# Kernel optimization log

Measured on AMD Instinct MI355X. Metric: run time of the kernel, lower is better.

Reference implementation:

```python
import jax, jax.numpy as jnp
import numpy as np

N_NODES = 20000
N_EDGES = 120000
N_GRAPHS = 512
F_IN = 300
NHID = 256
NHID_FF = 256
NOUT = 768
SLOPE = 0.2
EPS = 1e-16


def _p(key, shape, scale=0.05):
    return jax.random.normal(key, shape, dtype=jnp.float32) * scale


def setup_inputs() -> dict:
    key = jax.random.key(0)
    ks = jax.random.split(key, 24)
    inp = {
        "x": jax.random.normal(ks[0], (N_NODES, F_IN), dtype=jnp.float32),
        "edge_index": jax.random.randint(ks[1], (2, N_EDGES), 0, N_NODES, dtype=jnp.int64) if False else jax.random.randint(ks[1], (2, N_EDGES), 0, N_NODES).astype(jnp.int32),
        "batch": jnp.sort(jax.random.randint(ks[2], (N_NODES,), 0, N_GRAPHS)).astype(jnp.int32),
        # conv1: in=300 -> heads=4, C=256, concat
        "c1_wl": _p(ks[3], (4 * NHID, F_IN)),
        "c1_wr": _p(ks[4], (4 * NHID, F_IN)),
        "c1_att": _p(ks[5], (4, NHID)),
        "c1_b": jnp.zeros((4 * NHID,), jnp.float32),
        # conv2: in=1024 -> heads=4, C=256, concat
        "c2_wl": _p(ks[6], (4 * NHID, 4 * NHID)),
        "c2_wr": _p(ks[7], (4 * NHID, 4 * NHID)),
        "c2_att": _p(ks[8], (4, NHID)),
        "c2_b": jnp.zeros((4 * NHID,), jnp.float32),
        # conv3: in=1024 -> heads=6, C=256, mean (concat=False)
        "c3_wl": _p(ks[9], (6 * NHID_FF, 4 * NHID)),
        "c3_wr": _p(ks[10], (6 * NHID_FF, 4 * NHID)),
        "c3_att": _p(ks[11], (6, NHID_FF)),
        "c3_b": jnp.zeros((NHID_FF,), jnp.float32),
        # post-process MLP
        "fp1_w": _p(ks[12], (NHID_FF, NHID_FF)),
        "fp1_b": jnp.zeros((NHID_FF,), jnp.float32),
        "fp2_w": _p(ks[13], (NOUT, NHID_FF)),
        "fp2_b": jnp.zeros((NOUT,), jnp.float32),
    }
    return inp


def gatv2(x, src, dst, wl, wr, att, b, concat):
    """GATv2Conv (PyG semantics, eval mode): lin_l on source, lin_r on target,
    score = att . leaky_relu(xl_j + xr_i), segment softmax over dst, aggregate xl_j."""
    n = x.shape[0]
    H, C = att.shape
    xl = (x @ wl.T).reshape(n, H, C)
    xr = (x @ wr.T).reshape(n, H, C)
    s = xl[src] + xr[dst]                                   # [E,H,C] gather
    s = jnp.where(s > 0, s, SLOPE * s)                      # leaky_relu
    scores = jnp.einsum("ehc,hc->eh", s, att)               # [E,H]
    mx = jax.ops.segment_max(scores, dst, num_segments=n)   # [N,H]
    ex = jnp.exp(scores - mx[dst])
    denom = jax.ops.segment_sum(ex, dst, num_segments=n)
    alpha = ex / (denom[dst] + EPS)                         # [E,H]
    out = jax.ops.segment_sum(alpha[:, :, None] * xl[src], dst, num_segments=n)  # [N,H,C]
    out = out.reshape(n, H * C) if concat else out.mean(axis=1)
    return out + b


def reference(x, edge_index, batch, c1_wl, c1_wr, c1_att, c1_b,
              c2_wl, c2_wr, c2_att, c2_b, c3_wl, c3_wr, c3_att, c3_b,
              fp1_w, fp1_b, fp2_w, fp2_b):
    n = x.shape[0]
    # PyG GATv2Conv defaults add_self_loops=True
    loops = jnp.arange(n, dtype=edge_index.dtype)
    src = jnp.concatenate([edge_index[0], loops])
    dst = jnp.concatenate([edge_index[1], loops])

    h = jax.nn.elu(gatv2(x, src, dst, c1_wl, c1_wr, c1_att, c1_b, concat=True))
    h = jax.nn.elu(gatv2(h, src, dst, c2_wl, c2_wr, c2_att, c2_b, concat=True))
    h = gatv2(h, src, dst, c3_wl, c3_wr, c3_att, c3_b, concat=False)

    # F.normalize(p=2, dim=-1), torch eps=1e-12
    norm = jnp.linalg.norm(h, axis=-1, keepdims=True)
    h = h / jnp.maximum(norm, 1e-12)

    # global_mean_pool over `batch`
    sums = jax.ops.segment_sum(h, batch, num_segments=N_GRAPHS)
    cnts = jax.ops.segment_sum(jnp.ones((n,), h.dtype), batch, num_segments=N_GRAPHS)
    pooled = sums / jnp.maximum(cnts, 1.0)[:, None]

    h = jax.nn.relu(pooled @ fp1_w.T + fp1_b)
    return h @ fp2_w.T + fp2_b
```

## Files before the change

### kernel.cpp

```cpp
#include <hip/hip_runtime.h>

typedef _Float16 h16;
typedef _Float16 h16x4 __attribute__((ext_vector_type(4)));
typedef _Float16 h16x8 __attribute__((ext_vector_type(8)));
typedef float f32x4 __attribute__((ext_vector_type(4)));

static constexpr int NN   = 20000;
static constexpr int NPAD = 20096;
static constexpr int NE0  = 120000;
static constexpr int NE   = 140000;
static constexpr int NG   = 512;
static constexpr int FIN  = 300;
static constexpr int K1P  = 320;
static constexpr int CD   = 256;
static constexpr float SLOPE = 0.2f;

#define GLDS16(gsrc, ldst)                                                              \
  __builtin_amdgcn_global_load_lds(                                                    \
      (const __attribute__((address_space(1))) unsigned int*)(gsrc),                    \
      (__attribute__((address_space(3))) unsigned int*)(ldst), 16, 0, 0)

__global__ __launch_bounds__(256) void fill_x_kernel(const float* __restrict__ x, h16* __restrict__ a1) {
  int r = blockIdx.x;
  for (int c = threadIdx.x; c < K1P; c += 256) {
    float v = (r < NN && c < FIN) ? x[(size_t)r * FIN + c] : 0.f;
    a1[(size_t)r * K1P + c] = (h16)v;
  }
}

__global__ __launch_bounds__(256) void conv_w2_kernel(const float* __restrict__ wl, const float* __restrict__ wr,
                                                      h16* __restrict__ o, int rows, int cols, int colsp) {
  int r = blockIdx.x;
  const float* s = (r < rows) ? (wl + (size_t)r * cols) : (wr + (size_t)(r - rows) * cols);
  for (int c = threadIdx.x; c < colsp; c += 256) {
    float v = (c < cols) ? s[c] : 0.f;
    o[(size_t)r * colsp + c] = (h16)v;
  }
}

__global__ __launch_bounds__(256) void build_edges_kernel(const int* __restrict__ ei,
                                                          int* __restrict__ src, int* __restrict__ dst) {
  int e = blockIdx.x * 256 + threadIdx.x;
  if (e >= NE) return;
  if (e < NE0) { src[e] = ei[e]; dst[e] = ei[NE0 + e]; }
  else         { src[e] = e - NE0; dst[e] = e - NE0; }
}

__global__ __launch_bounds__(256) void deg_kernel(const int* __restrict__ dst, int* __restrict__ deg) {
  int e = blockIdx.x * 256 + threadIdx.x;
  if (e < NE) atomicAdd(&deg[dst[e]], 1);
}

__global__ __launch_bounds__(1024) void scan_kernel(const int* __restrict__ deg, int* __restrict__ rowptr) {
  __shared__ int b0[1024], b1[1024];
  __shared__ int carry;
  int t = threadIdx.x;
  if (t == 0) carry = 0;
  __syncthreads();
  for (int base = 0; base < NN; base += 1024) {
    int x = (base + t < NN) ? deg[base + t] : 0;
    b0[t] = x;
    __syncthreads();
    int* cur = b0; int* nxt = b1;
    for (int off = 1; off < 1024; off <<= 1) {
      int v = cur[t];
      if (t >= off) v += cur[t - off];
      nxt[t] = v;
      __syncthreads();
      int* tmp = cur; cur = nxt; nxt = tmp;
    }
    if (base + t < NN) rowptr[base + t] = carry + cur[t] - x;
    __syncthreads();
    if (t == 0) carry += cur[1023];
    __syncthreads();
  }
  if (t == 0) rowptr[NN] = carry;
}

__global__ __launch_bounds__(256) void scatter_kernel(const int* __restrict__ src, const int* __restrict__ dst,
                                                      const int* __restrict__ rowptr, int* __restrict__ cursor,
                                                      int* __restrict__ esrc) {
  int e = blockIdx.x * 256 + threadIdx.x;
  if (e >= NE) return;
  int d = dst[e];
  int pos = rowptr[d] + atomicAdd(&cursor[d], 1);
  esrc[pos] = src[e];
}

__global__ __launch_bounds__(256) void gemm_kernel(const h16* __restrict__ A, const h16* __restrict__ B,
                                                   h16* __restrict__ Co, int K, int Nw, int ntN) {
  __shared__ __align__(16) h16 As[128 * 32];
  __shared__ __align__(16) h16 Bs[128 * 32];
  int nwg = gridDim.x;
  int q = nwg >> 3, r = nwg & 7;
  int xc = blockIdx.x & 7, idx = blockIdx.x >> 3;
  int logical = (xc < r ? xc * (q + 1) : r * (q + 1) + (xc - r) * q) + idx;
  int tm = (logical / ntN) * 128, tn = (logical % ntN) * 128;

  int tid = threadIdx.x, w = tid >> 6, lane = tid & 63;
  int wm = (w >> 1) * 64, wn = (w & 1) * 64;
  const h16* gA = A + (size_t)(tm + w * 16 + (lane >> 2)) * K + (lane & 3) * 8;
  const h16* gB = B + (size_t)(tn + w * 16 + (lane >> 2)) * K + (lane & 3) * 8;
  h16* lA0 = As + w * 512;
  h16* lA1 = As + 2048 + w * 512;
  h16* lB0 = Bs + w * 512;
  h16* lB1 = Bs + 2048 + w * 512;
  const size_t rowskip = (size_t)64 * K;
  int lrow = lane & 15, kg = (lane >> 4) * 8;

  f32x4 acc[4][4] = {};
  for (int k0 = 0; k0 < K; k0 += 32) {
    __syncthreads();
    GLDS16(gA + k0, lA0);
    GLDS16(gA + rowskip + k0, lA1);
    GLDS16(gB + k0, lB0);
    GLDS16(gB + rowskip + k0, lB1);
    __syncthreads();
    h16x8 af[4], bf[4];
#pragma unroll
    for (int i = 0; i < 4; i++) af[i] = *(const h16x8*)&As[(wm + i * 16 + lrow) * 32 + kg];
#pragma unroll
    for (int j = 0; j < 4; j++) bf[j] = *(const h16x8*)&Bs[(wn + j * 16 + lrow) * 32 + kg];
#pragma unroll
    for (int i = 0; i < 4; i++)
#pragma unroll
      for (int j = 0; j < 4; j++)
        acc[i][j] = __builtin_amdgcn_mfma_f32_16x16x32_f16(af[i], bf[j], acc[i][j], 0, 0, 0);
  }
  int cr = (lane >> 4) * 4, cc = lane & 15;
#pragma unroll
  for (int i = 0; i < 4; i++)
#pragma unroll
    for (int j = 0; j < 4; j++) {
      size_t base = (size_t)(tm + wm + i * 16 + cr) * Nw + (tn + wn + j * 16 + cc);
#pragma unroll
      for (int qq = 0; qq < 4; qq++) Co[base + (size_t)qq * Nw] = (h16)acc[i][j][qq];
    }
}

template <int H, int MODE>
__global__ __launch_bounds__(64 * H) void sagg_kernel(
    const h16* __restrict__ X, const int* __restrict__ rowptr, const int* __restrict__ esrc,
    const float* __restrict__ att, const float* __restrict__ bias,
    h16* __restrict__ outA, const int* __restrict__ batch,
    float* __restrict__ pooled, int* __restrict__ cnt) {
  constexpr int HC = H * CD, S = 2 * HC;
  int n = blockIdx.x;
  int tid = threadIdx.x, w = tid >> 6, lane = tid & 63;
  int cb = w * CD + lane * 4;

  float4 aw4 = *(const float4*)(att + cb);
  const float* aw = (const float*)&aw4;
  h16x4 xr4 = *(const h16x4*)(X + (size_t)n * S + HC + cb);
  float xr0 = (float)xr4[0], xr1 = (float)xr4[1], xr2 = (float)xr4[2], xr3 = (float)xr4[3];

  int beg = rowptr[n], end = rowptr[n + 1];
  float m = -1e30f, s = 0.f;
  float a0 = 0.f, a1 = 0.f, a2 = 0.f, a3 = 0.f;
  for (int i = beg; i < end; ++i) {
    int j = esrc[i];
    h16x4 xl4 = *(const h16x4*)(X + (size_t)j * S + cb);
    float x0 = (float)xl4[0], x1 = (float)xl4[1], x2 = (float)xl4[2], x3 = (float)xl4[3];
    float v0 = x0 + xr0, v1 = x1 + xr1, v2 = x2 + xr2, v3 = x3 + xr3;
    v0 = v0 > 0.f ? v0 : SLOPE * v0;
    v1 = v1 > 0.f ? v1 : SLOPE * v1;
    v2 = v2 > 0.f ? v2 : SLOPE * v2;
    v3 = v3 > 0.f ? v3 : SLOPE * v3;
    float p = v0 * aw[0] + v1 * aw[1] + v2 * aw[2] + v3 * aw[3];
    p += __shfl_xor(p, 32); p += __shfl_xor(p, 16); p += __shfl_xor(p, 8);
    p += __shfl_xor(p, 4);  p += __shfl_xor(p, 2);  p += __shfl_xor(p, 1);
    float nm = fmaxf(m, p);
    float f = __expf(m - nm), we = __expf(p - nm);
    s = s * f + we;
    a0 = a0 * f + we * x0; a1 = a1 * f + we * x1;
    a2 = a2 * f + we * x2; a3 = a3 * f + we * x3;
    m = nm;
  }
  float inv = 1.f / (s + 1e-16f);

  if (MODE == 0) {
    float o0 = a0 * inv + bias[cb + 0];
    float o1 = a1 * inv + bias[cb + 1];
    float o2 = a2 * inv + bias[cb + 2];
    float o3 = a3 * inv + bias[cb + 3];
    o0 = o0 > 0.f ? o0 : expm1f(o0);
    o1 = o1 > 0.f ? o1 : expm1f(o1);
    o2 = o2 > 0.f ? o2 : expm1f(o2);
    o3 = o3 > 0.f ? o3 : expm1f(o3);
    h16x4 ov = {(h16)o0, (h16)o1, (h16)o2, (h16)o3};
    *(h16x4*)(outA + (size_t)n * HC + cb) = ov;
  } else {
    __shared__ float sh[HC];
    __shared__ float red[H];
    float4 nv = {a0 * inv, a1 * inv, a2 * inv, a3 * inv};
    *(float4*)&sh[cb] = nv;
    __syncthreads();
    float mv = 0.f;
    if (tid < CD) {
#pragma unroll
      for (int h = 0; h < H; h++) mv += sh[h * CD + tid];
      mv = mv * (1.f / H) + bias[tid];
    }
    float ss = (tid < CD) ? mv * mv : 0.f;
    ss += __shfl_xor(ss, 32); ss += __shfl_xor(ss, 16); ss += __shfl_xor(ss, 8);
    ss += __shfl_xor(ss, 4);  ss += __shfl_xor(ss, 2);  ss += __shfl_xor(ss, 1);
    if (lane == 0) red[w] = ss;
    __syncthreads();
    float tot = 0.f;
#pragma unroll
    for (int h = 0; h < H; h++) tot += red[h];
    float scale = 1.f / fmaxf(sqrtf(tot), 1e-12f);
    int g = batch[n];
    if (tid < CD) atomicAdd(&pooled[(size_t)g * CD + tid], mv * scale);
    if (tid == 0) atomicAdd(&cnt[g], 1);
  }
}

__global__ __launch_bounds__(256) void pool_div_kernel(float* __restrict__ pooled, const int* __restrict__ cnt) {
  int g = blockIdx.x, t = threadIdx.x;
  pooled[(size_t)g * CD + t] /= fmaxf((float)cnt[g], 1.f);
}

__global__ __launch_bounds__(256) void mlp1_kernel(const float* __restrict__ pooled, const float* __restrict__ w,
                                                   const float* __restrict__ b, float* __restrict__ hid) {
  __shared__ float xs[CD];
  int g = blockIdx.x, t = threadIdx.x;
  xs[t] = pooled[(size_t)g * CD + t];
  __syncthreads();
  float acc = b[t];
  for (int k = 0; k < CD; ++k) acc += xs[k] * w[(size_t)t * CD + k];
  hid[(size_t)g * CD + t] = fmaxf(acc, 0.f);
}

__global__ __launch_bounds__(256) void mlp2_kernel(const float* __restrict__ hid, const float* __restrict__ w,
                                                   const float* __restrict__ b, float* __restrict__ out) {
  __shared__ float xs[CD];
  int g = blockIdx.x, t = threadIdx.x;
  xs[t] = hid[(size_t)g * CD + t];
  __syncthreads();
  for (int o = t; o < 768; o += 256) {
    float acc = b[o];
    for (int k = 0; k < CD; ++k) acc += xs[k] * w[(size_t)o * CD + k];
    out[(size_t)g * 768 + o] = acc;
  }
}

extern "C" void kernel_launch(void* const* d_in, const int* in_sizes, int n_in,
                              void* d_out, int out_size, void* d_ws, size_t ws_size,
                              hipStream_t stream) {
  const float* x      = (const float*)d_in[0];
  const int*   ei     = (const int*)d_in[1];
  const int*   batch  = (const int*)d_in[2];
  const float* c1_wl  = (const float*)d_in[3];
  const float* c1_wr  = (const float*)d_in[4];
  const float* c1_att = (const float*)d_in[5];
  const float* c1_b   = (const float*)d_in[6];
  const float* c2_wl  = (const float*)d_in[7];
  const float* c2_wr  = (const float*)d_in[8];
  const float* c2_att = (const float*)d_in[9];
  const float* c2_b   = (const float*)d_in[10];
  const float* c3_wl  = (const float*)d_in[11];
  const float* c3_wr  = (const float*)d_in[12];
  const float* c3_att = (const float*)d_in[13];
  const float* c3_b   = (const float*)d_in[14];
  const float* fp1_w  = (const float*)d_in[15];
  const float* fp1_b  = (const float*)d_in[16];
  const float* fp2_w  = (const float*)d_in[17];
  const float* fp2_b  = (const float*)d_in[18];

  char* p = (char*)d_ws;
  size_t off = 0;
  auto alloc = [&](size_t b) { void* r = p + off; off += (b + 255) & ~(size_t)255; return r; };
  h16*  A    = (h16*)alloc((size_t)NPAD * 1024 * 2);
  h16*  Xa   = (h16*)alloc((size_t)NPAD * 3072 * 2);
  h16*  Xb   = (h16*)alloc((size_t)NPAD * 2048 * 2);
  h16*  A1   = Xb;
  h16*  W1   = (h16*)alloc((size_t)2048 * K1P * 2);
  h16*  W2   = (h16*)alloc((size_t)2048 * 1024 * 2);
  h16*  W3   = (h16*)alloc((size_t)3072 * 1024 * 2);
  int*  srcA   = (int*)alloc((size_t)NE * 4);
  int*  dstA   = (int*)alloc((size_t)NE * 4);
  int*  esrc   = (int*)alloc((size_t)NE * 4);
  int*  deg    = (int*)alloc((size_t)NN * 4);
  int*  cursor = (int*)alloc((size_t)NN * 4);
  int*  rowptr = (int*)alloc((size_t)(NN + 1) * 4);
  float* pooled = (float*)alloc((size_t)NG * CD * 4);
  int*  cnt    = (int*)alloc((size_t)NG * 4);
  float* hid   = (float*)alloc((size_t)NG * CD * 4);

  hipMemsetAsync(deg, 0, (size_t)NN * 4, stream);
  hipMemsetAsync(cursor, 0, (size_t)NN * 4, stream);
  hipMemsetAsync(pooled, 0, (size_t)NG * CD * 4, stream);
  hipMemsetAsync(cnt, 0, (size_t)NG * 4, stream);

  fill_x_kernel<<<NPAD, 256, 0, stream>>>(x, A1);
  conv_w2_kernel<<<2048, 256, 0, stream>>>(c1_wl, c1_wr, W1, 1024, FIN, K1P);
  conv_w2_kernel<<<2048, 256, 0, stream>>>(c2_wl, c2_wr, W2, 1024, 1024, 1024);
  conv_w2_kernel<<<3072, 256, 0, stream>>>(c3_wl, c3_wr, W3, 1536, 1024, 1024);

  int eb = (NE + 255) / 256;
  build_edges_kernel<<<eb, 256, 0, stream>>>(ei, srcA, dstA);
  deg_kernel<<<eb, 256, 0, stream>>>(dstA, deg);
  scan_kernel<<<1, 1024, 0, stream>>>(deg, rowptr);
  scatter_kernel<<<eb, 256, 0, stream>>>(srcA, dstA, rowptr, cursor, esrc);

  gemm_kernel<<<157 * 16, 256, 0, stream>>>(A1, W1, Xa, K1P, 2048, 16);
  sagg_kernel<4, 0><<<NN, 256, 0, stream>>>(Xa, rowptr, esrc, c1_att, c1_b, A, nullptr, nullptr, nullptr);

  gemm_kernel<<<157 * 16, 256, 0, stream>>>(A, W2, Xb, 1024, 2048, 16);
  sagg_kernel<4, 0><<<NN, 256, 0, stream>>>(Xb, rowptr, esrc, c2_att, c2_b, A, nullptr, nullptr, nullptr);

  gemm_kernel<<<157 * 24, 256, 0, stream>>>(A, W3, Xa, 1024, 3072, 24);
  sagg_kernel<6, 1><<<NN, 384, 0, stream>>>(Xa, rowptr, esrc, c3_att, c3_b, nullptr, batch, pooled, cnt);

  pool_div_kernel<<<NG, 256, 0, stream>>>(pooled, cnt);
  mlp1_kernel<<<NG, 256, 0, stream>>>(pooled, fp1_w, fp1_b, hid);
  mlp2_kernel<<<NG, 256, 0, stream>>>(hid, fp2_w, fp2_b, (float*)d_out);
}
```

Measured before the change: 777.4 us.

## Use 256x256 double-buffered swizzled GEMM tiles and batch neighbor gathers in aggregation

Replaces the 128x128 single-buffered GEMM with a 256x256-tile, 512-thread kernel. It uses K-step 64, double-buffered LDS via global_load_lds, an XOR swizzle against bank conflicts, and explicit waitcnt and barrier control so loads overlap the MFMAs. Padding grows (K1P to 384, NPAD to 20224) to fit the larger tiles. The aggregation kernels now prefetch up to 8 neighbor indices and feature rows before the online-softmax loop, exposing memory-level parallelism in the edge gather. The larger tiles cut global and LDS traffic per MFMA but raise register and LDS pressure (128KB of LDS per block) and do extra padded work.

```diff
diff --git a/kernel.cpp b/kernel.cpp
--- a/kernel.cpp
+++ b/kernel.cpp
@@ -6,12 +6,12 @@
 typedef float f32x4 __attribute__((ext_vector_type(4)));
 
 static constexpr int NN   = 20000;
-static constexpr int NPAD = 20096;
+static constexpr int NPAD = 20224;
 static constexpr int NE0  = 120000;
 static constexpr int NE   = 140000;
 static constexpr int NG   = 512;
 static constexpr int FIN  = 300;
-static constexpr int K1P  = 320;
+static constexpr int K1P  = 384;
 static constexpr int CD   = 256;
 static constexpr float SLOPE = 0.2f;
 
@@ -87,51 +87,80 @@
   esrc[pos] = src[e];
 }
 
-__global__ __launch_bounds__(256) void gemm_kernel(const h16* __restrict__ A, const h16* __restrict__ B,
-                                                   h16* __restrict__ Co, int K, int Nw, int ntN) {
-  __shared__ __align__(16) h16 As[128 * 32];
-  __shared__ __align__(16) h16 Bs[128 * 32];
+__global__ __launch_bounds__(512, 2) void gemm256_kernel(const h16* __restrict__ A, const h16* __restrict__ B,
+                                                         h16* __restrict__ Co, int K, int Nw, int ntN) {
+  __shared__ __align__(16) h16 lds[4 * 16384];
   int nwg = gridDim.x;
   int q = nwg >> 3, r = nwg & 7;
   int xc = blockIdx.x & 7, idx = blockIdx.x >> 3;
   int logical = (xc < r ? xc * (q + 1) : r * (q + 1) + (xc - r) * q) + idx;
-  int tm = (logical / ntN) * 128, tn = (logical % ntN) * 128;
-
-  int tid = threadIdx.x, w = tid >> 6, lane = tid & 63;
-  int wm = (w >> 1) * 64, wn = (w & 1) * 64;
-  const h16* gA = A + (size_t)(tm + w * 16 + (lane >> 2)) * K + (lane & 3) * 8;
-  const h16* gB = B + (size_t)(tn + w * 16 + (lane >> 2)) * K + (lane & 3) * 8;
-  h16* lA0 = As + w * 512;
-  h16* lA1 = As + 2048 + w * 512;
-  h16* lB0 = Bs + w * 512;
-  h16* lB1 = Bs + 2048 + w * 512;
-  const size_t rowskip = (size_t)64 * K;
-  int lrow = lane & 15, kg = (lane >> 4) * 8;
-
-  f32x4 acc[4][4] = {};
-  for (int k0 = 0; k0 < K; k0 += 32) {
-    __syncthreads();
-    GLDS16(gA + k0, lA0);
-    GLDS16(gA + rowskip + k0, lA1);
-    GLDS16(gB + k0, lB0);
-    GLDS16(gB + rowskip + k0, lB1);
-    __syncthreads();
-    h16x8 af[4], bf[4];
-#pragma unroll
-    for (int i = 0; i < 4; i++) af[i] = *(const h16x8*)&As[(wm + i * 16 + lrow) * 32 + kg];
-#pragma unroll
-    for (int j = 0; j < 4; j++) bf[j] = *(const h16x8*)&Bs[(wn + j * 16 + lrow) * 32 + kg];
-#pragma unroll
-    for (int i = 0; i < 4; i++)
-#pragma unroll
-      for (int j = 0; j < 4; j++)
+  int tm = (logical / ntN) * 256, tn = (logical % ntN) * 256;
+
+  int tid = threadIdx.x;
+  int wv = tid >> 6, lane = tid & 63;
+  int wm = (wv >> 2) * 128, wn = (wv & 3) * 64;
+  int lrow = lane & 15, kq = lane >> 4, lr7 = lrow & 7;
+
+  int rowoff = tid >> 3;
+  int ug = ((tid & 7) ^ (rowoff & 7)) * 8;
+  int ldsoff = (tid >> 6) * 512;
+
+  const int NT = K >> 6;
+
+  auto STAGE = [&](int buf, int kt) {
+#pragma unroll
+    for (int j = 0; j < 4; ++j) {
+      GLDS16(A + (size_t)(tm + j * 64 + rowoff) * K + kt * 64 + ug,
+             &lds[(buf * 2 + 0) * 16384 + j * 4096 + ldsoff]);
+      GLDS16(B + (size_t)(tn + j * 64 + rowoff) * K + kt * 64 + ug,
+             &lds[(buf * 2 + 1) * 16384 + j * 4096 + ldsoff]);
+    }
+  };
+
+  STAGE(0, 0);
+  STAGE(1, 1);
+
+  f32x4 acc[8][4] = {};
+  for (int t = 0; t < NT; ++t) {
+    int b = t & 1;
+    if (t + 1 < NT) { asm volatile("s_waitcnt vmcnt(8)" ::: "memory"); }
+    else            { asm volatile("s_waitcnt vmcnt(0)" ::: "memory"); }
+    __builtin_amdgcn_s_barrier();
+
+    const h16* As_ = &lds[(b * 2 + 0) * 16384];
+    const h16* Bs_ = &lds[(b * 2 + 1) * 16384];
+    h16x8 af[8], bf[4];
+#pragma unroll
+    for (int i = 0; i < 8; ++i) af[i] = *(const h16x8*)&As_[(wm + i * 16 + lrow) * 64 + ((kq ^ lr7) * 8)];
+#pragma unroll
+    for (int j = 0; j < 4; ++j) bf[j] = *(const h16x8*)&Bs_[(wn + j * 16 + lrow) * 64 + ((kq ^ lr7) * 8)];
+#pragma unroll
+    for (int i = 0; i < 8; ++i)
+#pragma unroll
+      for (int j = 0; j < 4; ++j)
         acc[i][j] = __builtin_amdgcn_mfma_f32_16x16x32_f16(af[i], bf[j], acc[i][j], 0, 0, 0);
-  }
-  int cr = (lane >> 4) * 4, cc = lane & 15;
-#pragma unroll
-  for (int i = 0; i < 4; i++)
-#pragma unroll
-    for (int j = 0; j < 4; j++) {
+#pragma unroll
+    for (int i = 0; i < 8; ++i) af[i] = *(const h16x8*)&As_[(wm + i * 16 + lrow) * 64 + (((4 + kq) ^ lr7) * 8)];
+#pragma unroll
+    for (int j = 0; j < 4; ++j) bf[j] = *(const h16x8*)&Bs_[(wn + j * 16 + lrow) * 64 + (((4 + kq) ^ lr7) * 8)];
+    asm volatile("s_waitcnt lgkmcnt(0)" ::: "memory");
+    __builtin_amdgcn_sched_barrier(0);
+    __builtin_amdgcn_s_barrier();
+    if (t + 2 < NT) STAGE(b, t + 2);
+    __builtin_amdgcn_s_setprio(1);
+#pragma unroll
+    for (int i = 0; i < 8; ++i)
+#pragma unroll
+      for (int j = 0; j < 4; ++j)
+        acc[i][j] = __builtin_amdgcn_mfma_f32_16x16x32_f16(af[i], bf[j], acc[i][j], 0, 0, 0);
+    __builtin_amdgcn_s_setprio(0);
+  }
+
+  int cr = kq * 4, cc = lrow;
+#pragma unroll
+  for (int i = 0; i < 8; ++i)
+#pragma unroll
+    for (int j = 0; j < 4; ++j) {
       size_t base = (size_t)(tm + wm + i * 16 + cr) * Nw + (tn + wn + j * 16 + cc);
 #pragma unroll
       for (int qq = 0; qq < 4; qq++) Co[base + (size_t)qq * Nw] = (h16)acc[i][j][qq];
@@ -157,24 +186,36 @@
   int beg = rowptr[n], end = rowptr[n + 1];
   float m = -1e30f, s = 0.f;
   float a0 = 0.f, a1 = 0.f, a2 = 0.f, a3 = 0.f;
-  for (int i = beg; i < end; ++i) {
-    int j = esrc[i];
-    h16x4 xl4 = *(const h16x4*)(X + (size_t)j * S + cb);
-    float x0 = (float)xl4[0], x1 = (float)xl4[1], x2 = (float)xl4[2], x3 = (float)xl4[3];
-    float v0 = x0 + xr0, v1 = x1 + xr1, v2 = x2 + xr2, v3 = x3 + xr3;
-    v0 = v0 > 0.f ? v0 : SLOPE * v0;
-    v1 = v1 > 0.f ? v1 : SLOPE * v1;
-    v2 = v2 > 0.f ? v2 : SLOPE * v2;
-    v3 = v3 > 0.f ? v3 : SLOPE * v3;
-    float p = v0 * aw[0] + v1 * aw[1] + v2 * aw[2] + v3 * aw[3];
-    p += __shfl_xor(p, 32); p += __shfl_xor(p, 16); p += __shfl_xor(p, 8);
-    p += __shfl_xor(p, 4);  p += __shfl_xor(p, 2);  p += __shfl_xor(p, 1);
-    float nm = fmaxf(m, p);
-    float f = __expf(m - nm), we = __expf(p - nm);
-    s = s * f + we;
-    a0 = a0 * f + we * x0; a1 = a1 * f + we * x1;
-    a2 = a2 * f + we * x2; a3 = a3 * f + we * x3;
-    m = nm;
+  int i = beg;
+  while (i < end) {
+    int cn = end - i; if (cn > 8) cn = 8;
+    int js[8];
+    h16x4 xs[8];
+#pragma unroll
+    for (int k = 0; k < 8; ++k) js[k] = esrc[i + (k < cn ? k : cn - 1)];
+#pragma unroll
+    for (int k = 0; k < 8; ++k) xs[k] = *(const h16x4*)(X + (size_t)js[k] * S + cb);
+#pragma unroll
+    for (int k = 0; k < 8; ++k) {
+      if (k < cn) {
+        float x0 = (float)xs[k][0], x1 = (float)xs[k][1], x2 = (float)xs[k][2], x3 = (float)xs[k][3];
+        float v0 = x0 + xr0, v1 = x1 + xr1, v2 = x2 + xr2, v3 = x3 + xr3;
+        v0 = v0 > 0.f ? v0 : SLOPE * v0;
+        v1 = v1 > 0.f ? v1 : SLOPE * v1;
+        v2 = v2 > 0.f ? v2 : SLOPE * v2;
+        v3 = v3 > 0.f ? v3 : SLOPE * v3;
+        float p = v0 * aw[0] + v1 * aw[1] + v2 * aw[2] + v3 * aw[3];
+        p += __shfl_xor(p, 32); p += __shfl_xor(p, 16); p += __shfl_xor(p, 8);
+        p += __shfl_xor(p, 4);  p += __shfl_xor(p, 2);  p += __shfl_xor(p, 1);
+        float nm = fmaxf(m, p);
+        float f = __expf(m - nm), we = __expf(p - nm);
+        s = s * f + we;
+        a0 = a0 * f + we * x0; a1 = a1 * f + we * x1;
+        a2 = a2 * f + we * x2; a3 = a3 * f + we * x3;
+        m = nm;
+      }
+    }
+    i += cn;
   }
   float inv = 1.f / (s + 1e-16f);
 
@@ -304,13 +345,13 @@
   scan_kernel<<<1, 1024, 0, stream>>>(deg, rowptr);
   scatter_kernel<<<eb, 256, 0, stream>>>(srcA, dstA, rowptr, cursor, esrc);
 
-  gemm_kernel<<<157 * 16, 256, 0, stream>>>(A1, W1, Xa, K1P, 2048, 16);
+  gemm256_kernel<<<79 * 8, 512, 0, stream>>>(A1, W1, Xa, K1P, 2048, 8);
   sagg_kernel<4, 0><<<NN, 256, 0, stream>>>(Xa, rowptr, esrc, c1_att, c1_b, A, nullptr, nullptr, nullptr);
 
-  gemm_kernel<<<157 * 16, 256, 0, stream>>>(A, W2, Xb, 1024, 2048, 16);
+  gemm256_kernel<<<79 * 8, 512, 0, stream>>>(A, W2, Xb, 1024, 2048, 8);
   sagg_kernel<4, 0><<<NN, 256, 0, stream>>>(Xb, rowptr, esrc, c2_att, c2_b, A, nullptr, nullptr, nullptr);
 
-  gemm_kernel<<<157 * 24, 256, 0, stream>>>(A, W3, Xa, 1024, 3072, 24);
+  gemm256_kernel<<<79 * 12, 512, 0, stream>>>(A, W3, Xa, 1024, 3072, 12);
   sagg_kernel<6, 1><<<NN, 384, 0, stream>>>(Xa, rowptr, esrc, c3_att, c3_b, nullptr, batch, pooled, cnt);
 
   pool_div_kernel<<<NG, 256, 0, stream>>>(pooled, cnt);
```

New measurement: 726.0 us. 1.07x faster.
